# Optimization experiments

Measured on AMD Instinct MI355X. Metric: run time of the kernel, lower is better.

The kernel has to match this reference:

```python
import jax, jax.numpy as jnp
import numpy as np

N, E, C0, H, NC = 50000, 800000, 64, 64, 2500
NUM_LAYERS = 3


def setup_inputs() -> dict:
    key = jax.random.key(0)
    ks = jax.random.split(key, 16)
    inp = {}
    inp["x"] = jax.random.normal(ks[0], (N, C0), dtype=jnp.float32)
    inp["edge_index"] = jax.random.randint(ks[1], (2, E), 0, N, dtype=jnp.int64)
    inp["cluster"] = jax.random.randint(ks[2], (N,), 0, NC, dtype=jnp.int64)
    c = C0
    for i in range(NUM_LAYERS):
        inp[f"w1_{i}"] = jax.random.normal(ks[3 + 4 * i], (c, H), jnp.float32) / np.sqrt(c).astype(np.float32)
        inp[f"b1_{i}"] = jnp.zeros((H,), jnp.float32)
        inp[f"w2_{i}"] = jax.random.normal(ks[4 + 4 * i], (H, c), jnp.float32) / np.sqrt(H).astype(np.float32)
        inp[f"b2_{i}"] = jnp.zeros((c,), jnp.float32)
        c *= 2
    inp["n_clusters"] = NC
    return inp


def _glp(x, src, dst, w1, b1, w2, b2, num_nodes):
    # node encoder MLP: Linear -> ReLU -> Linear
    h = jnp.maximum(x @ w1 + b1, 0.0) @ w2 + b2  # [N, c]
    # message passing: gather at source, scatter-max at destination
    msg = h[src]  # [E, c]
    aggr = jax.ops.segment_max(msg, dst, num_segments=num_nodes)  # [N, c]
    # nodes with no incoming edges -> 0 (PyG fill for max aggregation)
    aggr = jnp.where(jnp.isfinite(aggr), aggr, 0.0)
    # update: concat(encoder_out, aggregated) -> channels double
    return jnp.concatenate([h, aggr], axis=1)


def reference(x, edge_index, cluster,
              w1_0, b1_0, w2_0, b2_0,
              w1_1, b1_1, w2_1, b2_1,
              w1_2, b1_2, w2_2, b2_2,
              n_clusters):
    num_nodes = x.shape[0]
    src, dst = edge_index[0], edge_index[1]
    params = [(w1_0, b1_0, w2_0, b2_0), (w1_1, b1_1, w2_1, b2_1), (w1_2, b1_2, w2_2, b2_2)]
    for (w1, b1, w2, b2) in params:
        x = _glp(x, src, dst, w1, b1, w2, b2, num_nodes)
    # cluster-wise max pool over polylines
    pooled = jax.ops.segment_max(x, cluster, num_segments=n_clusters)  # [NC, 512]
    pooled = jnp.where(jnp.isfinite(pooled), pooled, 0.0)
    # column-wise (dim=0) normalization as in the source
    out = pooled / (jnp.linalg.norm(pooled, axis=0) + 1e-6)
    return out
```

## Files before the change

### kernel.cpp

```cpp
#include <hip/hip_runtime.h>
#include <math.h>

typedef unsigned short bfu;
typedef __attribute__((ext_vector_type(8))) short bf16x8;
typedef __attribute__((ext_vector_type(16))) float f32x16;

__device__ __forceinline__ float b2f(bfu u) {
    unsigned int x = ((unsigned int)u) << 16;
    return __uint_as_float(x);
}
__device__ __forceinline__ bfu f2bf(float f) {
    unsigned int u = __float_as_uint(f);
    unsigned int r = (u + 0x7FFFu + ((u >> 16) & 1u)) >> 16;
    return (bfu)r;
}

struct InitArgs {
    int* deg; int N; int* cdeg; int NC; float* sumsq;
    const float* w[6]; bfu* whi[6]; bfu* wlo[6]; int K[6]; int Nw[6];
    const float* x0; bfu* xhi; bfu* xlo; int xtotal;
};

__global__ __launch_bounds__(256) void k_init(InitArgs a) {
    const int j = blockIdx.y;
    const int g0 = blockIdx.x * 256 + threadIdx.x;
    const int gs = gridDim.x * 256;
    if (j == 0) {
        for (int i = g0; i < a.N; i += gs) a.deg[i] = 0;
        for (int i = g0; i < a.NC; i += gs) a.cdeg[i] = 0;
        for (int i = g0; i < 512; i += gs) a.sumsq[i] = 0.f;
    } else if (j <= 6) {
        const int jj = j - 1;
        const int K = a.K[jj], Nw = a.Nw[jj];
        const int total = K * Nw;
        const float* w = a.w[jj];
        bfu* dhi = a.whi[jj];
        bfu* dlo = a.wlo[jj];
        for (int idx = g0; idx < total; idx += gs) {
            int k = idx / Nw, n = idx % Nw;
            float v = w[idx];
            bfu hi = f2bf(v);
            bfu lo = f2bf(v - b2f(hi));
            dhi[n * K + k] = hi;
            dlo[n * K + k] = lo;
        }
    } else {
        for (int i = g0; i * 4 < a.xtotal; i += gs) {
            int base = i * 4;
            float4 v = *(const float4*)&a.x0[base];
            ushort4 h, l;
            h.x = f2bf(v.x); l.x = f2bf(v.x - b2f(h.x));
            h.y = f2bf(v.y); l.y = f2bf(v.y - b2f(h.y));
            h.z = f2bf(v.z); l.z = f2bf(v.z - b2f(h.z));
            h.w = f2bf(v.w); l.w = f2bf(v.w - b2f(h.w));
            *(ushort4*)&a.xhi[base] = h;
            *(ushort4*)&a.xlo[base] = l;
        }
    }
}

__global__ void k_hist2(const int* __restrict__ dst, int E, int* __restrict__ deg,
                        const int* __restrict__ cluster, int N, int* __restrict__ cdeg) {
    int i = blockIdx.x * blockDim.x + threadIdx.x;
    if (i < E) atomicAdd(&deg[dst[i]], 1);
    if (i < N) atomicAdd(&cdeg[cluster[i]], 1);
}

__global__ __launch_bounds__(256) void k_scanA(const int* __restrict__ deg, int N,
                                               const int* __restrict__ cdeg, int NC,
                                               int* __restrict__ scn0, int* __restrict__ scn1,
                                               int* __restrict__ bsum0, int* __restrict__ bsum1) {
    __shared__ int part[256];
    const int seg = blockIdx.y;
    const int n = seg ? NC : N;
    const int* d = seg ? cdeg : deg;
    int* scn = seg ? scn1 : scn0;
    int* bs  = seg ? bsum1 : bsum0;
    const int b = blockIdx.x;
    if (b * 256 >= n) return;
    const int t = threadIdx.x;
    const int i = b * 256 + t;
    int v = (i < n) ? d[i] : 0;
    part[t] = v;
    __syncthreads();
#pragma unroll
    for (int off = 1; off < 256; off <<= 1) {
        int cv = part[t];
        int u = (t >= off) ? part[t - off] : 0;
        __syncthreads();
        part[t] = cv + u;
        __syncthreads();
    }
    if (i < n) scn[i] = part[t];
    if (t == 255) bs[b] = part[255];
}

__global__ __launch_bounds__(256) void k_scanB(int* __restrict__ bsum0, int nb0,
                                               int* __restrict__ bsum1, int nb1,
                                               int* __restrict__ ptr0, int N,
                                               int* __restrict__ ptr1, int NC) {
    __shared__ int part[256];
    const int t = threadIdx.x;
    int v = (t < nb0) ? bsum0[t] : 0;
    part[t] = v;
    __syncthreads();
#pragma unroll
    for (int off = 1; off < 256; off <<= 1) {
        int cv = part[t];
        int u = (t >= off) ? part[t - off] : 0;
        __syncthreads();
        part[t] = cv + u;
        __syncthreads();
    }
    if (t < nb0) bsum0[t] = part[t] - v;
    if (t == 255) ptr0[N] = part[255];
    __syncthreads();
    v = (t < nb1) ? bsum1[t] : 0;
    part[t] = v;
    __syncthreads();
#pragma unroll
    for (int off = 1; off < 256; off <<= 1) {
        int cv = part[t];
        int u = (t >= off) ? part[t - off] : 0;
        __syncthreads();
        part[t] = cv + u;
        __syncthreads();
    }
    if (t < nb1) bsum1[t] = part[t] - v;
    if (t == 255) ptr1[NC] = part[255];
}

__global__ __launch_bounds__(256) void k_scanC(const int* __restrict__ deg, int N,
                                               const int* __restrict__ cdeg, int NC,
                                               const int* __restrict__ scn0, const int* __restrict__ scn1,
                                               const int* __restrict__ bsum0, const int* __restrict__ bsum1,
                                               int* __restrict__ ptr0, int* __restrict__ cur0,
                                               int* __restrict__ ptr1, int* __restrict__ cur1) {
    const int seg = blockIdx.y;
    const int n = seg ? NC : N;
    const int* d = seg ? cdeg : deg;
    const int* scn = seg ? scn1 : scn0;
    const int* bs  = seg ? bsum1 : bsum0;
    int* ptr = seg ? ptr1 : ptr0;
    int* cur = seg ? cur1 : cur0;
    const int b = blockIdx.x;
    if (b * 256 >= n) return;
    const int i = b * 256 + threadIdx.x;
    if (i < n) {
        int e = bs[b] + scn[i] - d[i];
        ptr[i] = e;
        cur[i] = e;
    }
}

__global__ void k_scatter2(const int* __restrict__ dst, const int* __restrict__ src, int E,
                           int* __restrict__ cur, int* __restrict__ colidx,
                           const int* __restrict__ cluster, int N,
                           int* __restrict__ ccur, int* __restrict__ cidx) {
    int i = blockIdx.x * blockDim.x + threadIdx.x;
    if (i < E) {
        int d = dst[i];
        int pos = atomicAdd(&cur[d], 1);
        colidx[pos] = src[i];
    }
    if (i < N) {
        int c = cluster[i];
        int pos = atomicAdd(&ccur[c], 1);
        cidx[pos] = i;
    }
}

__device__ __forceinline__ int swz(int row, int kb) {
    return (row * 128 + (kb ^ ((row & 7) << 4))) >> 1;
}

template <bool RELU, bool WLO>
__global__ __launch_bounds__(256) void k_gmfma(const bfu* __restrict__ Ahi, const bfu* __restrict__ Alo,
                                               const bfu* __restrict__ Bhi, const bfu* __restrict__ Blo,
                                               const float* __restrict__ bias,
                                               bfu* __restrict__ Ohi, bfu* __restrict__ Olo,
                                               int M, int K, int OS, int Kzero) {
    __shared__ __align__(16) bfu As[2][128 * 64];
    __shared__ __align__(16) bfu Bs[2][64 * 64];
    const int tid = threadIdx.x;
    const int wave = tid >> 6, lane = tid & 63;
    const int m0 = blockIdx.x * 128;
    const int n0 = blockIdx.y * 64;
    const int l31 = lane & 31;
    const int khalfb = (lane >> 5) * 16;

    f32x16 acc0, acc1;
#pragma unroll
    for (int i = 0; i < 16; i++) { acc0[i] = 0.f; acc1[i] = 0.f; }

    for (int k0 = 0; k0 < K; k0 += 64) {
        const bool full3 = (k0 < Kzero);
#pragma unroll
        for (int i = 0; i < 4; i++) {
            int idx = i * 2048 + tid * 8;
            int row = idx >> 6;
            int ke = idx & 63;
            int gm = m0 + row; if (gm >= M) gm = M - 1;
            uint4 v = *(const uint4*)&Ahi[(size_t)gm * K + k0 + ke];
            *(uint4*)&As[0][swz(row, ke * 2)] = v;
        }
        if (full3) {
#pragma unroll
            for (int i = 0; i < 4; i++) {
                int idx = i * 2048 + tid * 8;
                int row = idx >> 6;
                int ke = idx & 63;
                int gm = m0 + row; if (gm >= M) gm = M - 1;
                uint4 v = *(const uint4*)&Alo[(size_t)gm * K + k0 + ke];
                *(uint4*)&As[1][swz(row, ke * 2)] = v;
            }
        }
#pragma unroll
        for (int p = 0; p < 2; p++) {
            const bfu* src = p ? Blo : Bhi;
#pragma unroll
            for (int i = 0; i < 2; i++) {
                int idx = i * 2048 + tid * 8;
                int row = idx >> 6;
                int ke = idx & 63;
                uint4 v = *(const uint4*)&src[(size_t)(n0 + row) * K + k0 + ke];
                *(uint4*)&Bs[p][swz(row, ke * 2)] = v;
            }
        }
        __syncthreads();
        const int arow = wave * 32 + l31;
#pragma unroll
        for (int s = 0; s < 4; s++) {
            int kb = s * 32 + khalfb;
            bf16x8 ah = *(const bf16x8*)&As[0][swz(arow, kb)];
            bf16x8 bh0 = *(const bf16x8*)&Bs[0][swz(l31, kb)];
            bf16x8 bl0 = *(const bf16x8*)&Bs[1][swz(l31, kb)];
            bf16x8 bh1 = *(const bf16x8*)&Bs[0][swz(32 + l31, kb)];
            bf16x8 bl1 = *(const bf16x8*)&Bs[1][swz(32 + l31, kb)];
            acc0 = __builtin_amdgcn_mfma_f32_32x32x16_bf16(ah, bh0, acc0, 0, 0, 0);
            acc0 = __builtin_amdgcn_mfma_f32_32x32x16_bf16(ah, bl0, acc0, 0, 0, 0);
            acc1 = __builtin_amdgcn_mfma_f32_32x32x16_bf16(ah, bh1, acc1, 0, 0, 0);
            acc1 = __builtin_amdgcn_mfma_f32_32x32x16_bf16(ah, bl1, acc1, 0, 0, 0);
            if (full3) {
                bf16x8 al = *(const bf16x8*)&As[1][swz(arow, kb)];
                acc0 = __builtin_amdgcn_mfma_f32_32x32x16_bf16(al, bh0, acc0, 0, 0, 0);
                acc1 = __builtin_amdgcn_mfma_f32_32x32x16_bf16(al, bh1, acc1, 0, 0, 0);
            }
        }
        __syncthreads();
    }

    float bc0 = bias[n0 + l31];
    float bc1 = bias[n0 + 32 + l31];
    const int rbase = m0 + wave * 32 + 4 * (lane >> 5);
#pragma unroll
    for (int r = 0; r < 16; r++) {
        int grow = rbase + (r & 3) + 8 * (r >> 2);
        if (grow < M) {
            float o0 = acc0[r] + bc0;
            float o1 = acc1[r] + bc1;
            if (RELU) { o0 = fmaxf(o0, 0.f); o1 = fmaxf(o1, 0.f); }
            bfu h0 = f2bf(o0), h1 = f2bf(o1);
            size_t base = (size_t)grow * OS + n0;
            Ohi[base + l31] = h0;
            Ohi[base + 32 + l31] = h1;
            if (WLO) {
                Olo[base + l31] = f2bf(o0 - b2f(h0));
                Olo[base + 32 + l31] = f2bf(o1 - b2f(h1));
            }
        }
    }
}

template <int R>
__device__ __forceinline__ void gmax(const bfu* __restrict__ p, float* acc) {
    if (R == 4) {
        ushort4 v = *(const ushort4*)p;
        acc[0] = fmaxf(acc[0], b2f(v.x)); acc[1] = fmaxf(acc[1], b2f(v.y));
        acc[2] = fmaxf(acc[2], b2f(v.z)); acc[3] = fmaxf(acc[3], b2f(v.w));
    } else if (R == 2) {
        ushort2 v = *(const ushort2*)p;
        acc[0] = fmaxf(acc[0], b2f(v.x)); acc[1] = fmaxf(acc[1], b2f(v.y));
    } else {
        acc[0] = fmaxf(acc[0], b2f(*p));
    }
}

template <int R>
__global__ void k_agg(const bfu* __restrict__ hplane, bfu* __restrict__ whi,
                      const int* __restrict__ rowptr, const int* __restrict__ colidx,
                      int N, int stride) {
    const int w = (blockIdx.x * blockDim.x + threadIdx.x) >> 6;
    const int lane = threadIdx.x & 63;
    const int na = 2 * w, nb = na + 1;
    if (na >= N) return;
    const int ch = lane * R;
    const bool hasb = (nb < N);

    int bega = rowptr[na], enda = rowptr[na + 1];
    int begb = 0, endb = 0;
    if (hasb) { begb = rowptr[nb]; endb = rowptr[nb + 1]; }

    float acca[R], accb[R];
#pragma unroll
    for (int r = 0; r < R; r++) { acca[r] = -INFINITY; accb[r] = -INFINITY; }

    int ia = bega, ib = begb;
    while (ia + 4 <= enda && ib + 4 <= endb) {
        int offa[4], offb[4];
#pragma unroll
        for (int u = 0; u < 4; u++) {
            offa[u] = colidx[ia + u] * stride + ch;
            offb[u] = colidx[ib + u] * stride + ch;
        }
#pragma unroll
        for (int u = 0; u < 4; u++) {
            gmax<R>(hplane + offa[u], acca);
            gmax<R>(hplane + offb[u], accb);
        }
        ia += 4; ib += 4;
    }
    for (; ia + 4 <= enda; ia += 4) {
        int off[4];
#pragma unroll
        for (int u = 0; u < 4; u++) off[u] = colidx[ia + u] * stride + ch;
#pragma unroll
        for (int u = 0; u < 4; u++) gmax<R>(hplane + off[u], acca);
    }
    for (; ia < enda; ia++) gmax<R>(hplane + colidx[ia] * stride + ch, acca);
    for (; ib + 4 <= endb; ib += 4) {
        int off[4];
#pragma unroll
        for (int u = 0; u < 4; u++) off[u] = colidx[ib + u] * stride + ch;
#pragma unroll
        for (int u = 0; u < 4; u++) gmax<R>(hplane + off[u], accb);
    }
    for (; ib < endb; ib++) gmax<R>(hplane + colidx[ib] * stride + ch, accb);

    if (bega == enda) {
#pragma unroll
        for (int r = 0; r < R; r++) acca[r] = 0.f;
    }
    int obase = na * stride + 64 * R + ch;
#pragma unroll
    for (int r = 0; r < R; r++) whi[obase + r] = f2bf(acca[r]);

    if (hasb) {
        if (begb == endb) {
#pragma unroll
            for (int r = 0; r < R; r++) accb[r] = 0.f;
        }
        int obb = nb * stride + 64 * R + ch;
#pragma unroll
        for (int r = 0; r < R; r++) whi[obb + r] = f2bf(accb[r]);
    }
}

__global__ void k_pool(const bfu* __restrict__ xhi,
                       const int* __restrict__ cptr, const int* __restrict__ cidx,
                       float* __restrict__ pooled) {
    int cl = blockIdx.x;
    int tid = threadIdx.x;
    int beg = cptr[cl], end = cptr[cl + 1];
    float ax = -INFINITY, ay = -INFINITY;
    int i = beg;
    for (; i + 4 <= end; i += 4) {
        ushort2 h0 = *(const ushort2*)&xhi[cidx[i + 0] * 512 + tid * 2];
        ushort2 h1 = *(const ushort2*)&xhi[cidx[i + 1] * 512 + tid * 2];
        ushort2 h2 = *(const ushort2*)&xhi[cidx[i + 2] * 512 + tid * 2];
        ushort2 h3 = *(const ushort2*)&xhi[cidx[i + 3] * 512 + tid * 2];
        ax = fmaxf(ax, fmaxf(fmaxf(b2f(h0.x), b2f(h1.x)), fmaxf(b2f(h2.x), b2f(h3.x))));
        ay = fmaxf(ay, fmaxf(fmaxf(b2f(h0.y), b2f(h1.y)), fmaxf(b2f(h2.y), b2f(h3.y))));
    }
    for (; i < end; i++) {
        ushort2 h = *(const ushort2*)&xhi[cidx[i] * 512 + tid * 2];
        ax = fmaxf(ax, b2f(h.x)); ay = fmaxf(ay, b2f(h.y));
    }
    if (beg == end) { ax = 0.f; ay = 0.f; }
    float2 o; o.x = ax; o.y = ay;
    *(float2*)&pooled[(size_t)cl * 512 + tid * 2] = o;
}

__global__ void k_sumsq(const float* __restrict__ pooled, float* __restrict__ sumsq, int NC) {
    int tid = threadIdx.x;
    float ax = 0.f, ay = 0.f;
    for (int r = blockIdx.x; r < NC; r += gridDim.x) {
        float2 v = *(const float2*)&pooled[(size_t)r * 512 + tid * 2];
        ax += v.x * v.x; ay += v.y * v.y;
    }
    atomicAdd(&sumsq[tid * 2 + 0], ax);
    atomicAdd(&sumsq[tid * 2 + 1], ay);
}

__global__ void k_scale(const float* __restrict__ pooled, const float* __restrict__ sumsq,
                        float* __restrict__ out, int total) {
    int i = blockIdx.x * blockDim.x + threadIdx.x;
    int base = i * 4;
    if (base < total) {
        float4 v = *(const float4*)&pooled[base];
        int col = base & 511;
        v.x /= (sqrtf(sumsq[col + 0]) + 1e-6f);
        v.y /= (sqrtf(sumsq[col + 1]) + 1e-6f);
        v.z /= (sqrtf(sumsq[col + 2]) + 1e-6f);
        v.w /= (sqrtf(sumsq[col + 3]) + 1e-6f);
        *(float4*)&out[base] = v;
    }
}

extern "C" void kernel_launch(void* const* d_in, const int* in_sizes, int n_in,
                              void* d_out, int out_size, void* d_ws, size_t ws_size,
                              hipStream_t stream) {
    const float* x0      = (const float*)d_in[0];
    const int*   ei      = (const int*)d_in[1];
    const int*   cluster = (const int*)d_in[2];
    const float* w1_[3] = {(const float*)d_in[3], (const float*)d_in[7],  (const float*)d_in[11]};
    const float* b1_[3] = {(const float*)d_in[4], (const float*)d_in[8],  (const float*)d_in[12]};
    const float* w2_[3] = {(const float*)d_in[5], (const float*)d_in[9],  (const float*)d_in[13]};
    const float* b2_[3] = {(const float*)d_in[6], (const float*)d_in[10], (const float*)d_in[14]};

    const int N  = in_sizes[2];
    const int E  = in_sizes[1] / 2;
    const int NC = 2500;
    float* out = (float*)d_out;

    char* p = (char*)d_ws;
    auto alloc = [&](size_t bytes) -> char* {
        char* r = p;
        p += (bytes + 255) & ~(size_t)255;
        return r;
    };
    bfu* X0hi = (bfu*)alloc((size_t)N * 64 * 2);
    bfu* X0lo = (bfu*)alloc((size_t)N * 64 * 2);
    bfu* X1hi = (bfu*)alloc((size_t)N * 128 * 2);
    bfu* X1lo = (bfu*)alloc((size_t)N * 128 * 2);
    bfu* X2hi = (bfu*)alloc((size_t)N * 256 * 2);
    bfu* X2lo = (bfu*)alloc((size_t)N * 256 * 2);
    bfu* X3hi = (bfu*)alloc((size_t)N * 512 * 2);
    bfu* tbhi = (bfu*)alloc((size_t)N * 64 * 2);
    bfu* tblo = (bfu*)alloc((size_t)N * 64 * 2);
    bfu* w1t_hi[3]; bfu* w1t_lo[3]; bfu* w2t_hi[3]; bfu* w2t_lo[3];
    const int Ks[3] = {64, 128, 256};
    for (int l = 0; l < 3; l++) {
        w1t_hi[l] = (bfu*)alloc((size_t)64 * Ks[l] * 2);
        w1t_lo[l] = (bfu*)alloc((size_t)64 * Ks[l] * 2);
        w2t_hi[l] = (bfu*)alloc((size_t)Ks[l] * 64 * 2);
        w2t_lo[l] = (bfu*)alloc((size_t)Ks[l] * 64 * 2);
    }
    float* pooled = (float*)alloc((size_t)NC * 512 * 4);
    float* sumsq  = (float*)alloc(512 * 4);
    int*   deg    = (int*)alloc((size_t)(N + 1) * 4);
    int*   rowptr = (int*)alloc((size_t)(N + 1) * 4);
    int*   cursor = (int*)alloc((size_t)(N + 1) * 4);
    int*   colidx = (int*)alloc((size_t)E * 4);
    int*   cdeg   = (int*)alloc((size_t)(NC + 1) * 4);
    int*   cptr   = (int*)alloc((size_t)(NC + 1) * 4);
    int*   ccur   = (int*)alloc((size_t)(NC + 1) * 4);
    int*   cidx   = (int*)alloc((size_t)N * 4);
    int*   scn0   = (int*)alloc((size_t)N * 4);
    int*   scn1   = (int*)alloc((size_t)NC * 4);
    int*   bsum0  = (int*)alloc(256 * 4);
    int*   bsum1  = (int*)alloc(256 * 4);

    const int* src = ei;
    const int* dst = ei + E;

    InitArgs ia;
    ia.deg = deg; ia.N = N; ia.cdeg = cdeg; ia.NC = NC; ia.sumsq = sumsq;
    for (int l = 0; l < 3; l++) {
        ia.w[2 * l]     = w1_[l]; ia.whi[2 * l]     = w1t_hi[l]; ia.wlo[2 * l]     = w1t_lo[l];
        ia.K[2 * l]     = Ks[l];  ia.Nw[2 * l]      = 64;
        ia.w[2 * l + 1] = w2_[l]; ia.whi[2 * l + 1] = w2t_hi[l]; ia.wlo[2 * l + 1] = w2t_lo[l];
        ia.K[2 * l + 1] = 64;     ia.Nw[2 * l + 1]  = Ks[l];
    }
    ia.x0 = x0; ia.xhi = X0hi; ia.xlo = X0lo; ia.xtotal = N * 64;
    k_init<<<dim3(128, 8), 256, 0, stream>>>(ia);

    k_hist2<<<(E + 255) / 256, 256, 0, stream>>>(dst, E, deg, cluster, N, cdeg);

    const int nb0 = (N + 255) / 256;
    const int nb1 = (NC + 255) / 256;
    k_scanA<<<dim3(nb0, 2), 256, 0, stream>>>(deg, N, cdeg, NC, scn0, scn1, bsum0, bsum1);
    k_scanB<<<1, 256, 0, stream>>>(bsum0, nb0, bsum1, nb1, rowptr, N, cptr, NC);
    k_scanC<<<dim3(nb0, 2), 256, 0, stream>>>(deg, N, cdeg, NC, scn0, scn1, bsum0, bsum1,
                                              rowptr, cursor, cptr, ccur);

    k_scatter2<<<(E + 255) / 256, 256, 0, stream>>>(dst, src, E, cursor, colidx,
                                                    cluster, N, ccur, cidx);

    const int Mt = (N + 127) / 128;
    const int aggBlocks = (((N + 1) / 2) * 64 + 255) / 256;

    k_gmfma<true, true><<<dim3(Mt, 1), 256, 0, stream>>>(X0hi, X0lo, w1t_hi[0], w1t_lo[0], b1_[0], tbhi, tblo, N, 64, 64, 64);
    k_gmfma<false, true><<<dim3(Mt, 1), 256, 0, stream>>>(tbhi, tblo, w2t_hi[0], w2t_lo[0], b2_[0], X1hi, X1lo, N, 64, 128, 64);
    k_agg<1><<<aggBlocks, 256, 0, stream>>>(X1hi, X1hi, rowptr, colidx, N, 128);

    k_gmfma<true, true><<<dim3(Mt, 1), 256, 0, stream>>>(X1hi, X1lo, w1t_hi[1], w1t_lo[1], b1_[1], tbhi, tblo, N, 128, 64, 64);
    k_gmfma<false, true><<<dim3(Mt, 2), 256, 0, stream>>>(tbhi, tblo, w2t_hi[1], w2t_lo[1], b2_[1], X2hi, X2lo, N, 64, 256, 64);
    k_agg<2><<<aggBlocks, 256, 0, stream>>>(X2hi, X2hi, rowptr, colidx, N, 256);

    k_gmfma<true, true><<<dim3(Mt, 1), 256, 0, stream>>>(X2hi, X2lo, w1t_hi[2], w1t_lo[2], b1_[2], tbhi, tblo, N, 256, 64, 128);
    k_gmfma<false, false><<<dim3(Mt, 4), 256, 0, stream>>>(tbhi, tblo, w2t_hi[2], w2t_lo[2], b2_[2], X3hi, nullptr, N, 64, 512, 64);
    k_agg<4><<<aggBlocks, 256, 0, stream>>>(X3hi, X3hi, rowptr, colidx, N, 512);

    k_pool<<<NC, 256, 0, stream>>>(X3hi, cptr, cidx, pooled);
    k_sumsq<<<64, 256, 0, stream>>>(pooled, sumsq, NC);
    k_scale<<<(out_size / 4 + 255) / 256, 256, 0, stream>>>(pooled, sumsq, out, out_size);
}
```

Baseline: 335.2 us.

## Fuse per-layer MLP GEMMs, fold scan stage, one-node-per-wave aggregation

```diff
diff --git a/kernel.cpp b/kernel.cpp
--- a/kernel.cpp
+++ b/kernel.cpp
@@ -95,62 +95,44 @@
     if (t == 255) bs[b] = part[255];
 }
 
-__global__ __launch_bounds__(256) void k_scanB(int* __restrict__ bsum0, int nb0,
-                                               int* __restrict__ bsum1, int nb1,
-                                               int* __restrict__ ptr0, int N,
-                                               int* __restrict__ ptr1, int NC) {
-    __shared__ int part[256];
-    const int t = threadIdx.x;
-    int v = (t < nb0) ? bsum0[t] : 0;
-    part[t] = v;
-    __syncthreads();
-#pragma unroll
-    for (int off = 1; off < 256; off <<= 1) {
-        int cv = part[t];
-        int u = (t >= off) ? part[t - off] : 0;
-        __syncthreads();
-        part[t] = cv + u;
-        __syncthreads();
-    }
-    if (t < nb0) bsum0[t] = part[t] - v;
-    if (t == 255) ptr0[N] = part[255];
-    __syncthreads();
-    v = (t < nb1) ? bsum1[t] : 0;
-    part[t] = v;
-    __syncthreads();
-#pragma unroll
-    for (int off = 1; off < 256; off <<= 1) {
-        int cv = part[t];
-        int u = (t >= off) ? part[t - off] : 0;
-        __syncthreads();
-        part[t] = cv + u;
-        __syncthreads();
-    }
-    if (t < nb1) bsum1[t] = part[t] - v;
-    if (t == 255) ptr1[NC] = part[255];
-}
-
 __global__ __launch_bounds__(256) void k_scanC(const int* __restrict__ deg, int N,
                                                const int* __restrict__ cdeg, int NC,
                                                const int* __restrict__ scn0, const int* __restrict__ scn1,
-                                               const int* __restrict__ bsum0, const int* __restrict__ bsum1,
+                                               const int* __restrict__ bsum0, int nb0,
+                                               const int* __restrict__ bsum1, int nb1,
                                                int* __restrict__ ptr0, int* __restrict__ cur0,
                                                int* __restrict__ ptr1, int* __restrict__ cur1) {
+    __shared__ int part[256];
     const int seg = blockIdx.y;
     const int n = seg ? NC : N;
+    const int nb = seg ? nb1 : nb0;
     const int* d = seg ? cdeg : deg;
     const int* scn = seg ? scn1 : scn0;
-    const int* bs  = seg ? bsum1 : bsum0;
+    const int* bsum = seg ? bsum1 : bsum0;
     int* ptr = seg ? ptr1 : ptr0;
     int* cur = seg ? cur1 : cur0;
     const int b = blockIdx.x;
     if (b * 256 >= n) return;
-    const int i = b * 256 + threadIdx.x;
+    const int t = threadIdx.x;
+    int v = (t < nb) ? bsum[t] : 0;
+    part[t] = v;
+    __syncthreads();
+#pragma unroll
+    for (int off = 1; off < 256; off <<= 1) {
+        int cv = part[t];
+        int u = (t >= off) ? part[t - off] : 0;
+        __syncthreads();
+        part[t] = cv + u;
+        __syncthreads();
+    }
+    const int boff = (b == 0) ? 0 : part[b - 1];
+    const int i = b * 256 + t;
     if (i < n) {
-        int e = bs[b] + scn[i] - d[i];
+        int e = boff + scn[i] - d[i];
         ptr[i] = e;
         cur[i] = e;
     }
+    if (b == 0 && t == 0) ptr[n] = part[nb - 1];
 }
 
 __global__ void k_scatter2(const int* __restrict__ dst, const int* __restrict__ src, int E,
@@ -174,20 +156,22 @@
     return (row * 128 + (kb ^ ((row & 7) << 4))) >> 1;
 }
 
-template <bool RELU, bool WLO>
-__global__ __launch_bounds__(256) void k_gmfma(const bfu* __restrict__ Ahi, const bfu* __restrict__ Alo,
-                                               const bfu* __restrict__ Bhi, const bfu* __restrict__ Blo,
-                                               const float* __restrict__ bias,
+template <bool WLO>
+__global__ __launch_bounds__(256) void k_layer(const bfu* __restrict__ Ahi, const bfu* __restrict__ Alo,
+                                               const bfu* __restrict__ W1hi, const bfu* __restrict__ W1lo,
+                                               const float* __restrict__ b1,
+                                               const bfu* __restrict__ W2hi, const bfu* __restrict__ W2lo,
+                                               const float* __restrict__ b2,
                                                bfu* __restrict__ Ohi, bfu* __restrict__ Olo,
-                                               int M, int K, int OS, int Kzero) {
+                                               int M, int K, int Kzero, int Nw2, int OS) {
     __shared__ __align__(16) bfu As[2][128 * 64];
     __shared__ __align__(16) bfu Bs[2][64 * 64];
     const int tid = threadIdx.x;
     const int wave = tid >> 6, lane = tid & 63;
     const int m0 = blockIdx.x * 128;
-    const int n0 = blockIdx.y * 64;
     const int l31 = lane & 31;
     const int khalfb = (lane >> 5) * 16;
+    const int arow = wave * 32 + l31;
 
     f32x16 acc0, acc1;
 #pragma unroll
@@ -217,18 +201,17 @@
         }
 #pragma unroll
         for (int p = 0; p < 2; p++) {
-            const bfu* src = p ? Blo : Bhi;
+            const bfu* src = p ? W1lo : W1hi;
 #pragma unroll
             for (int i = 0; i < 2; i++) {
                 int idx = i * 2048 + tid * 8;
                 int row = idx >> 6;
                 int ke = idx & 63;
-                uint4 v = *(const uint4*)&src[(size_t)(n0 + row) * K + k0 + ke];
+                uint4 v = *(const uint4*)&src[(size_t)row * K + k0 + ke];
                 *(uint4*)&Bs[p][swz(row, ke * 2)] = v;
             }
         }
         __syncthreads();
-        const int arow = wave * 32 + l31;
 #pragma unroll
         for (int s = 0; s < 4; s++) {
             int kb = s * 32 + khalfb;
@@ -250,23 +233,74 @@
         __syncthreads();
     }
 
-    float bc0 = bias[n0 + l31];
-    float bc1 = bias[n0 + 32 + l31];
-    const int rbase = m0 + wave * 32 + 4 * (lane >> 5);
-#pragma unroll
-    for (int r = 0; r < 16; r++) {
-        int grow = rbase + (r & 3) + 8 * (r >> 2);
-        if (grow < M) {
-            float o0 = acc0[r] + bc0;
-            float o1 = acc1[r] + bc1;
-            if (RELU) { o0 = fmaxf(o0, 0.f); o1 = fmaxf(o1, 0.f); }
-            bfu h0 = f2bf(o0), h1 = f2bf(o1);
-            size_t base = (size_t)grow * OS + n0;
-            Ohi[base + l31] = h0;
-            Ohi[base + 32 + l31] = h1;
-            if (WLO) {
-                Olo[base + l31] = f2bf(o0 - b2f(h0));
-                Olo[base + 32 + l31] = f2bf(o1 - b2f(h1));
+    {
+        float bc0 = b1[l31];
+        float bc1 = b1[32 + l31];
+        const int rbase = wave * 32 + 4 * (lane >> 5);
+#pragma unroll
+        for (int r = 0; r < 16; r++) {
+            int row = rbase + (r & 3) + 8 * (r >> 2);
+            float t0 = fmaxf(acc0[r] + bc0, 0.f);
+            float t1 = fmaxf(acc1[r] + bc1, 0.f);
+            bfu h0 = f2bf(t0), h1 = f2bf(t1);
+            bfu l0 = f2bf(t0 - b2f(h0)), l1 = f2bf(t1 - b2f(h1));
+            As[0][swz(row, l31 * 2)] = h0;
+            As[0][swz(row, (32 + l31) * 2)] = h1;
+            As[1][swz(row, l31 * 2)] = l0;
+            As[1][swz(row, (32 + l31) * 2)] = l1;
+        }
+    }
+
+    for (int n0 = 0; n0 < Nw2; n0 += 64) {
+        __syncthreads();
+#pragma unroll
+        for (int p = 0; p < 2; p++) {
+            const bfu* src = p ? W2lo : W2hi;
+#pragma unroll
+            for (int i = 0; i < 2; i++) {
+                int idx = i * 2048 + tid * 8;
+                int row = idx >> 6;
+                int ke = idx & 63;
+                uint4 v = *(const uint4*)&src[(size_t)(n0 + row) * 64 + ke];
+                *(uint4*)&Bs[p][swz(row, ke * 2)] = v;
+            }
+        }
+        __syncthreads();
+#pragma unroll
+        for (int i = 0; i < 16; i++) { acc0[i] = 0.f; acc1[i] = 0.f; }
+#pragma unroll
+        for (int s = 0; s < 4; s++) {
+            int kb = s * 32 + khalfb;
+            bf16x8 th = *(const bf16x8*)&As[0][swz(arow, kb)];
+            bf16x8 tl = *(const bf16x8*)&As[1][swz(arow, kb)];
+            bf16x8 wh0 = *(const bf16x8*)&Bs[0][swz(l31, kb)];
+            bf16x8 wl0 = *(const bf16x8*)&Bs[1][swz(l31, kb)];
+            bf16x8 wh1 = *(const bf16x8*)&Bs[0][swz(32 + l31, kb)];
+            bf16x8 wl1 = *(const bf16x8*)&Bs[1][swz(32 + l31, kb)];
+            acc0 = __builtin_amdgcn_mfma_f32_32x32x16_bf16(th, wh0, acc0, 0, 0, 0);
+            acc0 = __builtin_amdgcn_mfma_f32_32x32x16_bf16(th, wl0, acc0, 0, 0, 0);
+            acc0 = __builtin_amdgcn_mfma_f32_32x32x16_bf16(tl, wh0, acc0, 0, 0, 0);
+            acc1 = __builtin_amdgcn_mfma_f32_32x32x16_bf16(th, wh1, acc1, 0, 0, 0);
+            acc1 = __builtin_amdgcn_mfma_f32_32x32x16_bf16(th, wl1, acc1, 0, 0, 0);
+            acc1 = __builtin_amdgcn_mfma_f32_32x32x16_bf16(tl, wh1, acc1, 0, 0, 0);
+        }
+        float bc0 = b2[n0 + l31];
+        float bc1 = b2[n0 + 32 + l31];
+        const int rbase = m0 + wave * 32 + 4 * (lane >> 5);
+#pragma unroll
+        for (int r = 0; r < 16; r++) {
+            int grow = rbase + (r & 3) + 8 * (r >> 2);
+            if (grow < M) {
+                float o0 = acc0[r] + bc0;
+                float o1 = acc1[r] + bc1;
+                bfu h0 = f2bf(o0), h1 = f2bf(o1);
+                size_t base = (size_t)grow * OS + n0;
+                Ohi[base + l31] = h0;
+                Ohi[base + 32 + l31] = h1;
+                if (WLO) {
+                    Olo[base + l31] = f2bf(o0 - b2f(h0));
+                    Olo[base + 32 + l31] = f2bf(o1 - b2f(h1));
+                }
             }
         }
     }
@@ -290,70 +324,39 @@
 __global__ void k_agg(const bfu* __restrict__ hplane, bfu* __restrict__ whi,
                       const int* __restrict__ rowptr, const int* __restrict__ colidx,
                       int N, int stride) {
-    const int w = (blockIdx.x * blockDim.x + threadIdx.x) >> 6;
+    const int wid = (blockIdx.x * blockDim.x + threadIdx.x) >> 6;
     const int lane = threadIdx.x & 63;
-    const int na = 2 * w, nb = na + 1;
-    if (na >= N) return;
+    if (wid >= N) return;
+    const int beg = rowptr[wid], end = rowptr[wid + 1];
     const int ch = lane * R;
-    const bool hasb = (nb < N);
-
-    int bega = rowptr[na], enda = rowptr[na + 1];
-    int begb = 0, endb = 0;
-    if (hasb) { begb = rowptr[nb]; endb = rowptr[nb + 1]; }
-
-    float acca[R], accb[R];
-#pragma unroll
-    for (int r = 0; r < R; r++) { acca[r] = -INFINITY; accb[r] = -INFINITY; }
-
-    int ia = bega, ib = begb;
-    while (ia + 4 <= enda && ib + 4 <= endb) {
-        int offa[4], offb[4];
-#pragma unroll
-        for (int u = 0; u < 4; u++) {
-            offa[u] = colidx[ia + u] * stride + ch;
-            offb[u] = colidx[ib + u] * stride + ch;
-        }
-#pragma unroll
-        for (int u = 0; u < 4; u++) {
-            gmax<R>(hplane + offa[u], acca);
-            gmax<R>(hplane + offb[u], accb);
-        }
-        ia += 4; ib += 4;
-    }
-    for (; ia + 4 <= enda; ia += 4) {
-        int off[4];
-#pragma unroll
-        for (int u = 0; u < 4; u++) off[u] = colidx[ia + u] * stride + ch;
-#pragma unroll
-        for (int u = 0; u < 4; u++) gmax<R>(hplane + off[u], acca);
-    }
-    for (; ia < enda; ia++) gmax<R>(hplane + colidx[ia] * stride + ch, acca);
-    for (; ib + 4 <= endb; ib += 4) {
-        int off[4];
-#pragma unroll
-        for (int u = 0; u < 4; u++) off[u] = colidx[ib + u] * stride + ch;
-#pragma unroll
-        for (int u = 0; u < 4; u++) gmax<R>(hplane + off[u], accb);
-    }
-    for (; ib < endb; ib++) gmax<R>(hplane + colidx[ib] * stride + ch, accb);
-
-    if (bega == enda) {
-#pragma unroll
-        for (int r = 0; r < R; r++) acca[r] = 0.f;
-    }
-    int obase = na * stride + 64 * R + ch;
-#pragma unroll
-    for (int r = 0; r < R; r++) whi[obase + r] = f2bf(acca[r]);
-
-    if (hasb) {
-        if (begb == endb) {
-#pragma unroll
-            for (int r = 0; r < R; r++) accb[r] = 0.f;
-        }
-        int obb = nb * stride + 64 * R + ch;
-#pragma unroll
-        for (int r = 0; r < R; r++) whi[obb + r] = f2bf(accb[r]);
-    }
+
+    float acc[R];
+#pragma unroll
+    for (int r = 0; r < R; r++) acc[r] = -INFINITY;
+
+    int i = beg;
+    for (; i + 8 <= end; i += 8) {
+        int off[8];
+#pragma unroll
+        for (int u = 0; u < 8; u++) off[u] = colidx[i + u] * stride + ch;
+#pragma unroll
+        for (int u = 0; u < 8; u++) gmax<R>(hplane + off[u], acc);
+    }
+    for (; i + 2 <= end; i += 2) {
+        int o0 = colidx[i] * stride + ch;
+        int o1 = colidx[i + 1] * stride + ch;
+        gmax<R>(hplane + o0, acc);
+        gmax<R>(hplane + o1, acc);
+    }
+    if (i < end) gmax<R>(hplane + colidx[i] * stride + ch, acc);
+
+    if (beg == end) {
+#pragma unroll
+        for (int r = 0; r < R; r++) acc[r] = 0.f;
+    }
+    int obase = wid * stride + 64 * R + ch;
+#pragma unroll
+    for (int r = 0; r < R; r++) whi[obase + r] = f2bf(acc[r]);
 }
 
 __global__ void k_pool(const bfu* __restrict__ xhi,
@@ -436,8 +439,6 @@
     bfu* X2hi = (bfu*)alloc((size_t)N * 256 * 2);
     bfu* X2lo = (bfu*)alloc((size_t)N * 256 * 2);
     bfu* X3hi = (bfu*)alloc((size_t)N * 512 * 2);
-    bfu* tbhi = (bfu*)alloc((size_t)N * 64 * 2);
-    bfu* tblo = (bfu*)alloc((size_t)N * 64 * 2);
     bfu* w1t_hi[3]; bfu* w1t_lo[3]; bfu* w2t_hi[3]; bfu* w2t_lo[3];
     const int Ks[3] = {64, 128, 256};
     for (int l = 0; l < 3; l++) {
@@ -480,26 +481,28 @@
     const int nb0 = (N + 255) / 256;
     const int nb1 = (NC + 255) / 256;
     k_scanA<<<dim3(nb0, 2), 256, 0, stream>>>(deg, N, cdeg, NC, scn0, scn1, bsum0, bsum1);
-    k_scanB<<<1, 256, 0, stream>>>(bsum0, nb0, bsum1, nb1, rowptr, N, cptr, NC);
-    k_scanC<<<dim3(nb0, 2), 256, 0, stream>>>(deg, N, cdeg, NC, scn0, scn1, bsum0, bsum1,
+    k_scanC<<<dim3(nb0, 2), 256, 0, stream>>>(deg, N, cdeg, NC, scn0, scn1, bsum0, nb0, bsum1, nb1,
                                               rowptr, cursor, cptr, ccur);
 
     k_scatter2<<<(E + 255) / 256, 256, 0, stream>>>(dst, src, E, cursor, colidx,
                                                     cluster, N, ccur, cidx);
 
     const int Mt = (N + 127) / 128;
-    const int aggBlocks = (((N + 1) / 2) * 64 + 255) / 256;
-
-    k_gmfma<true, true><<<dim3(Mt, 1), 256, 0, stream>>>(X0hi, X0lo, w1t_hi[0], w1t_lo[0], b1_[0], tbhi, tblo, N, 64, 64, 64);
-    k_gmfma<false, true><<<dim3(Mt, 1), 256, 0, stream>>>(tbhi, tblo, w2t_hi[0], w2t_lo[0], b2_[0], X1hi, X1lo, N, 64, 128, 64);
+    const int aggBlocks = (N * 64 + 255) / 256;
+
+    k_layer<true><<<Mt, 256, 0, stream>>>(X0hi, X0lo, w1t_hi[0], w1t_lo[0], b1_[0],
+                                          w2t_hi[0], w2t_lo[0], b2_[0], X1hi, X1lo,
+                                          N, 64, 64, 64, 128);
     k_agg<1><<<aggBlocks, 256, 0, stream>>>(X1hi, X1hi, rowptr, colidx, N, 128);
 
-    k_gmfma<true, true><<<dim3(Mt, 1), 256, 0, stream>>>(X1hi, X1lo, w1t_hi[1], w1t_lo[1], b1_[1], tbhi, tblo, N, 128, 64, 64);
-    k_gmfma<false, true><<<dim3(Mt, 2), 256, 0, stream>>>(tbhi, tblo, w2t_hi[1], w2t_lo[1], b2_[1], X2hi, X2lo, N, 64, 256, 64);
+    k_layer<true><<<Mt, 256, 0, stream>>>(X1hi, X1lo, w1t_hi[1], w1t_lo[1], b1_[1],
+                                          w2t_hi[1], w2t_lo[1], b2_[1], X2hi, X2lo,
+                                          N, 128, 64, 128, 256);
     k_agg<2><<<aggBlocks, 256, 0, stream>>>(X2hi, X2hi, rowptr, colidx, N, 256);
 
-    k_gmfma<true, true><<<dim3(Mt, 1), 256, 0, stream>>>(X2hi, X2lo, w1t_hi[2], w1t_lo[2], b1_[2], tbhi, tblo, N, 256, 64, 128);
-    k_gmfma<false, false><<<dim3(Mt, 4), 256, 0, stream>>>(tbhi, tblo, w2t_hi[2], w2t_lo[2], b2_[2], X3hi, nullptr, N, 64, 512, 64);
+    k_layer<false><<<Mt, 256, 0, stream>>>(X2hi, X2lo, w1t_hi[2], w1t_lo[2], b1_[2],
+                                           w2t_hi[2], w2t_lo[2], b2_[2], X3hi, nullptr,
+                                           N, 256, 128, 256, 512);
     k_agg<4><<<aggBlocks, 256, 0, stream>>>(X3hi, X3hi, rowptr, colidx, N, 512);
 
     k_pool<<<NC, 256, 0, stream>>>(X3hi, cptr, cidx, pooled);
```

New measurement: 303.5 us. 9.4% less time.
